# Kernel optimization log

Measured on AMD Instinct MI355X. Metric: run time of the kernel, lower is better.

Reference implementation:

```python
import jax, jax.numpy as jnp
import numpy as np

INPUT_DIM = 2048
N_EXPERTS = 64
K = 2


def setup_inputs() -> dict:
    key = jax.random.key(0)
    kx, kw, kb = jax.random.split(key, 3)
    x = jax.random.normal(kx, (4, 4096, INPUT_DIM), dtype=jnp.float32)
    # nn.Linear(input_dim, n_experts): weight [n_experts, input_dim], bias [n_experts]
    bound = 1.0 / np.sqrt(INPUT_DIM)
    W = jax.random.uniform(kw, (N_EXPERTS, INPUT_DIM), minval=-bound, maxval=bound, dtype=jnp.float32)
    b = jax.random.uniform(kb, (N_EXPERTS,), minval=-bound, maxval=bound, dtype=jnp.float32)
    return {"x": x, "W": W, "b": b}


def reference(x, W, b):
    # logits: [B, S, E]
    logits = jnp.einsum('bsd,ed->bse', x, W) + b
    topk_vals, topk_indices = jax.lax.top_k(logits, K)  # over last (expert) axis
    gate_probs = jax.nn.softmax(topk_vals, axis=-1)
    return gate_probs, topk_indices
```

## Files before the change

kernel.cpp:

```cpp
#include <hip/hip_runtime.h>
#include <math.h>
#include <stdint.h>

typedef _Float16 half8 __attribute__((ext_vector_type(8)));
typedef float floatx4 __attribute__((ext_vector_type(4)));

#define NTOK 16384
#define DIM  2048
#define NEXP 64
#define TPB  32
#define NBLK (NTOK / TPB)
#define KSPL 8
#define KW   (DIM / KSPL)
#define KC   32
#define NCH  (KW / KC)
#define WSW_H8 16384
#define WSW_BYTES (2 * WSW_H8 * 16)

#define SLOT_B  4096
#define WAVE_B  (2 * SLOT_B)
#define ARING_B (8 * WAVE_B)
#define FIN_F   (TPB * 65)

__global__ void wprep_kernel(const float* __restrict__ W, _Float16* __restrict__ wsw) {
    const int id   = blockIdx.x * blockDim.x + threadIdx.x;
    const int lane = id & 63;
    const int tg   = (id >> 6) & 3;
    const int sg   = id >> 8;
    const int e    = tg * 16 + (lane & 15);
    const int k    = sg * 32 + (lane >> 4) * 8;
    const float* src = W + (size_t)e * DIM + k;
    half8 h, l;
#pragma unroll
    for (int j = 0; j < 8; j++) {
        const float v  = src[j];
        const _Float16 hh = (_Float16)v;
        h[j] = hh;
        l[j] = (_Float16)((v - (float)hh) * 2048.0f);
    }
    const size_t slot = (size_t)(sg * 4 + tg) * 64 + lane;
    ((half8*)wsw)[slot]          = h;
    ((half8*)wsw)[WSW_H8 + slot] = l;
}

__device__ __forceinline__ void split_a(const float4& v0, const float4& v1,
                                        half8& hi, half8& lo) {
    const float av[8] = {v0.x, v0.y, v0.z, v0.w, v1.x, v1.y, v1.z, v1.w};
#pragma unroll
    for (int j = 0; j < 8; j++) {
        const _Float16 hh = (_Float16)av[j];
        hi[j] = hh;
        lo[j] = (_Float16)((av[j] - (float)hh) * 2048.0f);
    }
}

__device__ __forceinline__ void dma16(const void* g, const char* l) {
    __builtin_amdgcn_global_load_lds(
        (const __attribute__((address_space(1))) unsigned int*)(uintptr_t)g,
        (__attribute__((address_space(3))) unsigned int*)(uintptr_t)l,
        16, 0, 0);
}

template <int N>
__device__ __forceinline__ void wait_vm() {
    asm volatile("s_waitcnt vmcnt(%0)" :: "n"(N) : "memory");
}

template <bool USE_WS>
__global__ __launch_bounds__(512, 4)
void gating_kernel(const float* __restrict__ x, const float* __restrict__ W,
                   const _Float16* __restrict__ wsw, const float* __restrict__ bias,
                   float* __restrict__ out)
{
    __shared__ char  aring[ARING_B];
    __shared__ float fin[FIN_F];
    __shared__ float bsh[NEXP];

    const int tid  = threadIdx.x;
    const int lane = tid & 63;
    const int ks   = tid >> 6;
    const int col  = lane & 15;
    const int quad = lane >> 4;
    const int tok0 = blockIdx.x * TPB;

    if (tid < NEXP) bsh[tid] = bias[tid];

    const int arow = lane >> 3;
    const int agp  = (lane & 7) ^ arow;
    const float* gA = x + (size_t)(tok0 + arow) * DIM + ks * KW + agp * 4;
    char* const wbase = aring + ks * WAVE_B;

    floatx4 accm[2][4], accl[2][4];
#pragma unroll
    for (int m = 0; m < 2; m++)
#pragma unroll
        for (int t = 0; t < 4; t++) { accm[m][t] = (floatx4){0,0,0,0}; accl[m][t] = (floatx4){0,0,0,0}; }

#pragma unroll
    for (int i = 0; i < 4; i++)
        dma16(gA + (size_t)i * 8 * DIM, wbase + i * 1024);

#pragma unroll
    for (int c = 0; c < NCH; ++c) {
        const int sg = ks * NCH + c;
        half8  bh[4], bl[4];
        float4 bf0[4], bf1[4];
        if constexpr (USE_WS) {
#pragma unroll
            for (int t = 0; t < 4; t++) {
                bh[t] = ((const half8*)wsw)[(size_t)(sg * 4 + t) * 64 + lane];
                bl[t] = ((const half8*)wsw)[WSW_H8 + (size_t)(sg * 4 + t) * 64 + lane];
            }
        } else {
#pragma unroll
            for (int t = 0; t < 4; t++) {
                const float* wr = W + (size_t)(t * 16 + col) * DIM + sg * 32 + quad * 8;
                bf0[t] = *(const float4*)wr;
                bf1[t] = *(const float4*)(wr + 4);
            }
        }
        asm volatile("" ::: "memory");
        if (c + 1 < NCH) {
#pragma unroll
            for (int i = 0; i < 4; i++)
                dma16(gA + (size_t)i * 8 * DIM + (c + 1) * KC,
                      wbase + ((c + 1) & 1) * SLOT_B + i * 1024);
        }
        asm volatile("" ::: "memory");
        if (c + 1 < NCH) wait_vm<12>();
        else             wait_vm<8>();
        asm volatile("" ::: "memory");

        const char* Ab = wbase + (c & 1) * SLOT_B;
#pragma unroll
        for (int m = 0; m < 2; m++) {
            const int row = m * 16 + col;
            const float4 v0 = *(const float4*)(Ab + row * 128 + (((2 * quad + 0) ^ (row & 7))) * 16);
            const float4 v1 = *(const float4*)(Ab + row * 128 + (((2 * quad + 1) ^ (row & 7))) * 16);
            half8 ah, al;
            split_a(v0, v1, ah, al);
#pragma unroll
            for (int t = 0; t < 4; t++) {
                half8 hb, lb;
                if constexpr (USE_WS) { hb = bh[t]; lb = bl[t]; }
                else                  { split_a(bf0[t], bf1[t], hb, lb); }
                accm[m][t] = __builtin_amdgcn_mfma_f32_16x16x32_f16(ah, hb, accm[m][t], 0, 0, 0);
                accl[m][t] = __builtin_amdgcn_mfma_f32_16x16x32_f16(ah, lb, accl[m][t], 0, 0, 0);
                accl[m][t] = __builtin_amdgcn_mfma_f32_16x16x32_f16(al, hb, accl[m][t], 0, 0, 0);
            }
        }
    }

    __syncthreads();
    {
        float* slab = (float*)(aring + ks * WAVE_B);
        const float inv = 1.0f / 2048.0f;
#pragma unroll
        for (int m = 0; m < 2; m++)
#pragma unroll
            for (int t = 0; t < 4; t++)
#pragma unroll
                for (int r = 0; r < 4; r++)
                    slab[(m * 16 + quad * 4 + r) * 64 + t * 16 + col] =
                        accm[m][t][r] + accl[m][t][r] * inv;
    }
    __syncthreads();
    {
        const int tk = tid >> 4;
        const int e0 = (tid & 15) * 4;
        floatx4 s = {0, 0, 0, 0};
#pragma unroll
        for (int p = 0; p < KSPL; p++)
            s += *(const floatx4*)((const float*)(aring + p * WAVE_B) + tk * 64 + e0);
#pragma unroll
        for (int j = 0; j < 4; j++)
            fin[tk * 65 + e0 + j] = s[j] + bsh[e0 + j];
    }
    __syncthreads();

    if (tid < TPB) {
        const int tk = tid;
        float v0 = -INFINITY, v1 = -INFINITY;
        int   i0 = 0, i1 = 0;
        for (int e = 0; e < NEXP; e++) {
            const float v = fin[tk * 65 + e];
            if (v > v0)      { v1 = v0; i1 = i0; v0 = v; i0 = e; }
            else if (v > v1) { v1 = v; i1 = e; }
        }
        const float e1 = expf(v1 - v0);
        const float sden = 1.f + e1;
        const int   g  = tok0 + tk;
        out[2 * g + 0] = 1.f / sden;
        out[2 * g + 1] = e1 / sden;
        out[2 * NTOK + 2 * g + 0] = (float)i0;
        out[2 * NTOK + 2 * g + 1] = (float)i1;
    }
}

extern "C" void kernel_launch(void* const* d_in, const int* in_sizes, int n_in,
                              void* d_out, int out_size, void* d_ws, size_t ws_size,
                              hipStream_t stream) {
    const float* x    = (const float*)d_in[0];
    const float* W    = (const float*)d_in[1];
    const float* bias = (const float*)d_in[2];
    float*       out  = (float*)d_out;
    _Float16*    wsw  = (_Float16*)d_ws;

    if (ws_size >= (size_t)WSW_BYTES) {
        hipLaunchKernelGGL(wprep_kernel, dim3(64), dim3(256), 0, stream, W, wsw);
        hipLaunchKernelGGL((gating_kernel<true>), dim3(NBLK), dim3(512), 0, stream,
                           x, W, wsw, bias, out);
    } else {
        hipLaunchKernelGGL((gating_kernel<false>), dim3(NBLK), dim3(512), 0, stream,
                           x, W, nullptr, bias, out);
    }
}
```

Measured before the change: 208.4 us.

## Halve tokens per block, load whole A slice upfront, double-buffer weight fragments

Tokens per block drop from 32 to 16, which doubles the block count. Each wave now DMAs its entire 16x256 fp32 A slice into LDS in a single burst instead of streaming it through a two-slot ring. Weight fragments are register double-buffered so the next chunk's load overlaps the current chunk's MFMAs. LDS per block grows to 128KB and launch bounds drop to 2 blocks per CU, trading occupancy and weight reuse for fewer pipeline stalls and more parallelism.

```diff
diff --git a/kernel.cpp b/kernel.cpp
--- a/kernel.cpp
+++ b/kernel.cpp
@@ -8,7 +8,7 @@
 #define NTOK 16384
 #define DIM  2048
 #define NEXP 64
-#define TPB  32
+#define TPB  16
 #define NBLK (NTOK / TPB)
 #define KSPL 8
 #define KW   (DIM / KSPL)
@@ -17,8 +17,7 @@
 #define WSW_H8 16384
 #define WSW_BYTES (2 * WSW_H8 * 16)
 
-#define SLOT_B  4096
-#define WAVE_B  (2 * SLOT_B)
+#define WAVE_B  16384
 #define ARING_B (8 * WAVE_B)
 #define FIN_F   (TPB * 65)
 
@@ -66,8 +65,12 @@
     asm volatile("s_waitcnt vmcnt(%0)" :: "n"(N) : "memory");
 }
 
+__device__ __forceinline__ void fence_order() {
+    asm volatile("" ::: "memory");
+}
+
 template <bool USE_WS>
-__global__ __launch_bounds__(512, 4)
+__global__ __launch_bounds__(512, 2)
 void gating_kernel(const float* __restrict__ x, const float* __restrict__ W,
                    const _Float16* __restrict__ wsw, const float* __restrict__ bias,
                    float* __restrict__ out)
@@ -85,96 +88,101 @@
 
     if (tid < NEXP) bsh[tid] = bias[tid];
 
-    const int arow = lane >> 3;
-    const int agp  = (lane & 7) ^ arow;
-    const float* gA = x + (size_t)(tok0 + arow) * DIM + ks * KW + agp * 4;
     char* const wbase = aring + ks * WAVE_B;
 
-    floatx4 accm[2][4], accl[2][4];
-#pragma unroll
-    for (int m = 0; m < 2; m++)
-#pragma unroll
-        for (int t = 0; t < 4; t++) { accm[m][t] = (floatx4){0,0,0,0}; accl[m][t] = (floatx4){0,0,0,0}; }
-
-#pragma unroll
-    for (int i = 0; i < 4; i++)
-        dma16(gA + (size_t)i * 8 * DIM, wbase + i * 1024);
+    {
+        const float* rowp = x + (size_t)tok0 * DIM + ks * KW;
+#pragma unroll
+        for (int r = 0; r < TPB; r++)
+            dma16(rowp + (size_t)r * DIM + ((lane ^ (r & 7)) << 2),
+                  wbase + r * 1024);
+    }
+    fence_order();
+
+    floatx4 accm[4], accl[4];
+#pragma unroll
+    for (int t = 0; t < 4; t++) { accm[t] = (floatx4){0,0,0,0}; accl[t] = (floatx4){0,0,0,0}; }
+
+    half8  bh[2][4], bl[2][4];
+    float4 bf0[2][4], bf1[2][4];
+    if constexpr (USE_WS) {
+#pragma unroll
+        for (int t = 0; t < 4; t++) {
+            const size_t o = (size_t)((ks * NCH + 0) * 4 + t) * 64 + lane;
+            bh[0][t] = ((const half8*)wsw)[o];
+            bl[0][t] = ((const half8*)wsw)[WSW_H8 + o];
+        }
+    } else {
+#pragma unroll
+        for (int t = 0; t < 4; t++) {
+            const float* wr = W + (size_t)(t * 16 + col) * DIM + (ks * NCH) * 32 + quad * 8;
+            bf0[0][t] = *(const float4*)wr;
+            bf1[0][t] = *(const float4*)(wr + 4);
+        }
+    }
+    wait_vm<8>();
 
 #pragma unroll
     for (int c = 0; c < NCH; ++c) {
-        const int sg = ks * NCH + c;
-        half8  bh[4], bl[4];
-        float4 bf0[4], bf1[4];
-        if constexpr (USE_WS) {
-#pragma unroll
-            for (int t = 0; t < 4; t++) {
-                bh[t] = ((const half8*)wsw)[(size_t)(sg * 4 + t) * 64 + lane];
-                bl[t] = ((const half8*)wsw)[WSW_H8 + (size_t)(sg * 4 + t) * 64 + lane];
+        const int cur = c & 1, nxt = cur ^ 1;
+        if (c + 1 < NCH) {
+            if constexpr (USE_WS) {
+#pragma unroll
+                for (int t = 0; t < 4; t++) {
+                    const size_t o = (size_t)((ks * NCH + c + 1) * 4 + t) * 64 + lane;
+                    bh[nxt][t] = ((const half8*)wsw)[o];
+                    bl[nxt][t] = ((const half8*)wsw)[WSW_H8 + o];
+                }
+            } else {
+#pragma unroll
+                for (int t = 0; t < 4; t++) {
+                    const float* wr = W + (size_t)(t * 16 + col) * DIM + (ks * NCH + c + 1) * 32 + quad * 8;
+                    bf0[nxt][t] = *(const float4*)wr;
+                    bf1[nxt][t] = *(const float4*)(wr + 4);
+                }
             }
-        } else {
-#pragma unroll
-            for (int t = 0; t < 4; t++) {
-                const float* wr = W + (size_t)(t * 16 + col) * DIM + sg * 32 + quad * 8;
-                bf0[t] = *(const float4*)wr;
-                bf1[t] = *(const float4*)(wr + 4);
-            }
-        }
-        asm volatile("" ::: "memory");
-        if (c + 1 < NCH) {
-#pragma unroll
-            for (int i = 0; i < 4; i++)
-                dma16(gA + (size_t)i * 8 * DIM + (c + 1) * KC,
-                      wbase + ((c + 1) & 1) * SLOT_B + i * 1024);
-        }
-        asm volatile("" ::: "memory");
-        if (c + 1 < NCH) wait_vm<12>();
-        else             wait_vm<8>();
-        asm volatile("" ::: "memory");
-
-        const char* Ab = wbase + (c & 1) * SLOT_B;
-#pragma unroll
-        for (int m = 0; m < 2; m++) {
-            const int row = m * 16 + col;
-            const float4 v0 = *(const float4*)(Ab + row * 128 + (((2 * quad + 0) ^ (row & 7))) * 16);
-            const float4 v1 = *(const float4*)(Ab + row * 128 + (((2 * quad + 1) ^ (row & 7))) * 16);
-            half8 ah, al;
-            split_a(v0, v1, ah, al);
-#pragma unroll
-            for (int t = 0; t < 4; t++) {
-                half8 hb, lb;
-                if constexpr (USE_WS) { hb = bh[t]; lb = bl[t]; }
-                else                  { split_a(bf0[t], bf1[t], hb, lb); }
-                accm[m][t] = __builtin_amdgcn_mfma_f32_16x16x32_f16(ah, hb, accm[m][t], 0, 0, 0);
-                accl[m][t] = __builtin_amdgcn_mfma_f32_16x16x32_f16(ah, lb, accl[m][t], 0, 0, 0);
-                accl[m][t] = __builtin_amdgcn_mfma_f32_16x16x32_f16(al, hb, accl[m][t], 0, 0, 0);
-            }
+        }
+        const int pz0 = (c * 8 + quad * 2 + 0) ^ (col & 7);
+        const int pz1 = (c * 8 + quad * 2 + 1) ^ (col & 7);
+        const float4 v0 = *(const float4*)(wbase + col * 1024 + pz0 * 16);
+        const float4 v1 = *(const float4*)(wbase + col * 1024 + pz1 * 16);
+        half8 ah, al;
+        split_a(v0, v1, ah, al);
+#pragma unroll
+        for (int t = 0; t < 4; t++) {
+            half8 hb, lb;
+            if constexpr (USE_WS) { hb = bh[cur][t]; lb = bl[cur][t]; }
+            else                  { split_a(bf0[cur][t], bf1[cur][t], hb, lb); }
+            accm[t] = __builtin_amdgcn_mfma_f32_16x16x32_f16(ah, hb, accm[t], 0, 0, 0);
+            accl[t] = __builtin_amdgcn_mfma_f32_16x16x32_f16(ah, lb, accl[t], 0, 0, 0);
+            accl[t] = __builtin_amdgcn_mfma_f32_16x16x32_f16(al, hb, accl[t], 0, 0, 0);
         }
     }
 
     __syncthreads();
     {
-        float* slab = (float*)(aring + ks * WAVE_B);
+        float* slab = (float*)(aring + ks * 4096);
         const float inv = 1.0f / 2048.0f;
 #pragma unroll
-        for (int m = 0; m < 2; m++)
-#pragma unroll
-            for (int t = 0; t < 4; t++)
-#pragma unroll
-                for (int r = 0; r < 4; r++)
-                    slab[(m * 16 + quad * 4 + r) * 64 + t * 16 + col] =
-                        accm[m][t][r] + accl[m][t][r] * inv;
+        for (int t = 0; t < 4; t++)
+#pragma unroll
+            for (int r = 0; r < 4; r++)
+                slab[(quad * 4 + r) * 64 + t * 16 + col] =
+                    accm[t][r] + accl[t][r] * inv;
     }
     __syncthreads();
     {
-        const int tk = tid >> 4;
-        const int e0 = (tid & 15) * 4;
-        floatx4 s = {0, 0, 0, 0};
-#pragma unroll
-        for (int p = 0; p < KSPL; p++)
-            s += *(const floatx4*)((const float*)(aring + p * WAVE_B) + tk * 64 + e0);
-#pragma unroll
-        for (int j = 0; j < 4; j++)
-            fin[tk * 65 + e0 + j] = s[j] + bsh[e0 + j];
+        const int tk = tid >> 5;
+        const int e0 = (tid & 31) * 2;
+        float s0 = 0.f, s1 = 0.f;
+#pragma unroll
+        for (int p = 0; p < KSPL; p++) {
+            const float* sb = (const float*)(aring + p * 4096) + tk * 64 + e0;
+            s0 += sb[0];
+            s1 += sb[1];
+        }
+        fin[tk * 65 + e0]     = s0 + bsh[e0];
+        fin[tk * 65 + e0 + 1] = s1 + bsh[e0 + 1];
     }
     __syncthreads();
 
```

Result: slower. 227.1 us (+8.9%).
